# Kernel optimization log

Measured on AMD Instinct MI355X. Metric: run time of the kernel, lower is better.

The kernel has to match this reference:

```python
import jax, jax.numpy as jnp
import numpy as np

B, L, D, H, A = 4, 2048, 1024, 16, 64  # batch, seq, d_model, n_head, d_head


def setup_inputs() -> dict:
    key = jax.random.key(0)
    ks = jax.random.split(key, 6)
    scale = 1.0 / np.sqrt(D)
    return {
        "xq": jax.random.normal(ks[0], (B, L, D), dtype=jnp.float32),
        "xkv": jax.random.normal(ks[1], (B, L, D), dtype=jnp.float32),
        "Q": jax.random.normal(ks[2], (D, H, A), dtype=jnp.float32) * scale,
        "K": jax.random.normal(ks[3], (D, H, A), dtype=jnp.float32) * scale,
        "V": jax.random.normal(ks[4], (D, H, A), dtype=jnp.float32) * scale,
        "O": jax.random.normal(ks[5], (D, H, A), dtype=jnp.float32) * scale,
    }


def reference(xq, xkv, Q, K, V, O):
    # embed: 'dha, ...ld -> ...lha'
    q = jnp.einsum('dha,bld->blha', Q, xq)
    k = jnp.einsum('dha,bld->blha', K, xkv)
    v = jnp.einsum('dha,bld->blha', V, xkv)
    # outer: '...lha, ...mha -> ...hlm'  (full LxL score matrix, no scaling in source)
    scores = jnp.einsum('blha,bmha->bhlm', q, k)
    attn = jax.nn.softmax(scores, axis=-1)  # dropout p=0 (eval)
    # score: '...hlm, ...mha -> ...lha'
    ctx = jnp.einsum('bhlm,bmha->blha', attn, v)
    # output: '...dha, ...lha -> ...ld'
    return jnp.einsum('dha,blha->bld', O, ctx)
```

## Files before the change

### kernel.cpp

```cpp
#include <hip/hip_runtime.h>
#include <math.h>

typedef __bf16 bf16;
typedef bf16 bf16x8 __attribute__((ext_vector_type(8)));
typedef bf16 bf16x4 __attribute__((ext_vector_type(4)));
typedef float f32x4 __attribute__((ext_vector_type(4)));
typedef float f32x16 __attribute__((ext_vector_type(16)));

#define B_ 4
#define L_ 2048
#define D_ 1024
#define H_ 16
#define A_ 64
#define HA_ 1024
#define BL_ 8192
#define LOG2E 1.44269504088896340736f

__device__ __forceinline__ void gload16(const void* g, void* l) {
  __builtin_amdgcn_global_load_lds((const __attribute__((address_space(1))) void*)g,
                                   (__attribute__((address_space(3))) void*)l,
                                   16, 0, 0);
}

__device__ __forceinline__ unsigned cvt_pk_bf16(float lo, float hi) {
  unsigned r;
  asm volatile("v_cvt_pk_bf16_f32 %0, %1, %2" : "=v"(r) : "v"(lo), "v"(hi));
  return r;
}

__device__ __forceinline__ void permswap(unsigned& a, unsigned& b) {
  asm volatile("v_permlane32_swap_b32 %0, %1" : "+v"(a), "+v"(b));
}

__global__ __launch_bounds__(256) void cast_f32_bf16(const float* __restrict__ src,
                                                     bf16* __restrict__ dst, int n8) {
  int i = blockIdx.x * blockDim.x + threadIdx.x;
  if (i >= n8) return;
  const float4* s = reinterpret_cast<const float4*>(src) + (size_t)i * 2;
  float4 a = s[0], b = s[1];
  bf16x8 o;
  o[0] = (bf16)a.x; o[1] = (bf16)a.y; o[2] = (bf16)a.z; o[3] = (bf16)a.w;
  o[4] = (bf16)b.x; o[5] = (bf16)b.y; o[6] = (bf16)b.z; o[7] = (bf16)b.w;
  *reinterpret_cast<bf16x8*>(dst + (size_t)i * 8) = o;
}

__global__ __launch_bounds__(256) void transpose_cast_w(const float* __restrict__ w,
                                                        bf16* __restrict__ wt, float scale) {
  __shared__ float tile[32][33];
  const int d0 = blockIdx.y * 32, h0 = blockIdx.x * 32;
  const int tx = threadIdx.x, ty = threadIdx.y;
  #pragma unroll
  for (int j = 0; j < 4; j++)
    tile[ty + j * 8][tx] = w[(size_t)(d0 + ty + j * 8) * HA_ + h0 + tx];
  __syncthreads();
  #pragma unroll
  for (int j = 0; j < 4; j++)
    wt[(size_t)(h0 + ty + j * 8) * D_ + d0 + tx] = (bf16)(tile[tx][ty + j * 8] * scale);
}

__global__ __launch_bounds__(256) void transpose_v(const bf16* __restrict__ vb,
                                                   bf16* __restrict__ vtb) {
  __shared__ bf16 tile[64][72];
  const int bh = blockIdx.y;
  const int l0 = blockIdx.x * 64;
  const bf16* src = vb + (size_t)bh * L_ * A_ + (size_t)l0 * A_;
  bf16* dst = vtb + (size_t)bh * A_ * L_ + l0;
  const int tid = threadIdx.x;
  {
    int r = tid >> 2, cs = (tid & 3) * 16;
    bf16x8 v0 = *reinterpret_cast<const bf16x8*>(src + r * 64 + cs);
    bf16x8 v1 = *reinterpret_cast<const bf16x8*>(src + r * 64 + cs + 8);
    #pragma unroll
    for (int j = 0; j < 8; j++) { tile[r][cs + j] = v0[j]; tile[r][cs + 8 + j] = v1[j]; }
  }
  __syncthreads();
  {
    int a = tid >> 2, ls = (tid & 3) * 16;
    bf16x8 o0, o1;
    #pragma unroll
    for (int j = 0; j < 8; j++) { o0[j] = tile[ls + j][a]; o1[j] = tile[ls + 8 + j][a]; }
    *reinterpret_cast<bf16x8*>(dst + (size_t)a * L_ + ls) = o0;
    *reinterpret_cast<bf16x8*>(dst + (size_t)a * L_ + ls + 8) = o1;
  }
}

template <int MODE>
__device__ __forceinline__ void gemm_bt_core(const bf16* __restrict__ Ap,
                                             const bf16* __restrict__ Bp,
                                             void* __restrict__ Cp) {
  const int K = 1024;
  __shared__ __align__(16) bf16 As[128 * 32];
  __shared__ __align__(16) bf16 Bs[128 * 32];
  const int tid = threadIdx.x;
  const int m0 = blockIdx.y * 128, n0 = blockIdx.x * 128;
  const int lane = tid & 63, w = tid >> 6;
  const int wr = w >> 1, wc = w & 1;
  const int g = lane >> 4, c = lane & 15;
  f32x4 acc[4][4] = {};
  const int srow = tid >> 2, sch = tid & 3;
  const int sw0 = (sch ^ (srow & 3)) * 8;
  for (int k0 = 0; k0 < K; k0 += 32) {
    gload16(Ap + (size_t)(m0 + srow) * K + k0 + sw0, As + tid * 8);
    gload16(Ap + (size_t)(m0 + 64 + srow) * K + k0 + sw0, As + (256 + tid) * 8);
    gload16(Bp + (size_t)(n0 + srow) * K + k0 + sw0, Bs + tid * 8);
    gload16(Bp + (size_t)(n0 + 64 + srow) * K + k0 + sw0, Bs + (256 + tid) * 8);
    __syncthreads();
    bf16x8 af[4], bfr[4];
    #pragma unroll
    for (int m = 0; m < 4; m++)
      af[m] = *reinterpret_cast<const bf16x8*>(As + (wr * 64 + m * 16 + c) * 32 + ((g ^ (c & 3)) * 8));
    #pragma unroll
    for (int n = 0; n < 4; n++)
      bfr[n] = *reinterpret_cast<const bf16x8*>(Bs + (wc * 64 + n * 16 + c) * 32 + ((g ^ (c & 3)) * 8));
    #pragma unroll
    for (int m = 0; m < 4; m++)
      #pragma unroll
      for (int n = 0; n < 4; n++)
        acc[m][n] = __builtin_amdgcn_mfma_f32_16x16x32_bf16(af[m], bfr[n], acc[m][n], 0, 0, 0);
    __syncthreads();
  }
  #pragma unroll
  for (int m = 0; m < 4; m++) {
    #pragma unroll
    for (int n = 0; n < 4; n++) {
      #pragma unroll
      for (int i = 0; i < 4; i++) {
        int row = m0 + wr * 64 + m * 16 + g * 4 + i;
        int col = n0 + wc * 64 + n * 16 + c;
        float v = acc[m][n][i];
        if (MODE == 0) {
          int b = row >> 11, l = row & 2047, h = col >> 6, a = col & 63;
          ((bf16*)Cp)[(((size_t)b * H_ + h) * L_ + l) * A_ + a] = (bf16)v;
        } else {
          ((float*)Cp)[(size_t)row * 1024 + col] = v;
        }
      }
    }
  }
}

__global__ __launch_bounds__(256, 2) void gemm_proj(const bf16* xq_b, const bf16* xkv_b,
                                                    const bf16* wq, const bf16* wk, const bf16* wv,
                                                    bf16* qb, bf16* kb, bf16* vb) {
  const int z = blockIdx.z;
  const bf16* Ap = (z == 0) ? xq_b : xkv_b;
  const bf16* Bp = (z == 0) ? wq : (z == 1) ? wk : wv;
  bf16* Cp = (z == 0) ? qb : (z == 1) ? kb : vb;
  gemm_bt_core<0>(Ap, Bp, Cp);
}

__global__ __launch_bounds__(256, 2) void gemm_out_k(const bf16* ctx, const bf16* wo, float* out) {
  gemm_bt_core<1>(ctx, wo, out);
}

__device__ __forceinline__ void pa_build(const f32x16& s, bf16x8& f0, bf16x8& f1) {
  #pragma unroll
  for (int sl = 0; sl < 2; sl++) {
    unsigned a0 = cvt_pk_bf16(s[8 * sl + 0], s[8 * sl + 1]);
    unsigned b0 = cvt_pk_bf16(s[8 * sl + 4], s[8 * sl + 5]);
    permswap(a0, b0);
    unsigned a1 = cvt_pk_bf16(s[8 * sl + 2], s[8 * sl + 3]);
    unsigned b1 = cvt_pk_bf16(s[8 * sl + 6], s[8 * sl + 7]);
    permswap(a1, b1);
    uint4 v; v.x = a0; v.y = a1; v.z = b0; v.w = b1;
    if (sl == 0) f0 = __builtin_bit_cast(bf16x8, v);
    else         f1 = __builtin_bit_cast(bf16x8, v);
  }
}

__global__ __launch_bounds__(512, 2) void attn_kernel(const bf16* __restrict__ qg,
                                                      const bf16* __restrict__ kg,
                                                      const bf16* __restrict__ vtg,
                                                      bf16* __restrict__ ctx) {
  __shared__ __align__(16) bf16 Ks[2][64 * 64];
  __shared__ __align__(16) bf16 Vs[2][64 * 64];
  const int tid = threadIdx.x;
  const int lane = tid & 63;
  const int w = tid >> 6;
  const int c = lane & 31;
  const int hi = lane >> 5;
  const int cs7 = c & 7;
  const int bh = blockIdx.y;
  const int q0 = blockIdx.x * 256;
  const bf16* qh = qg + (size_t)bh * L_ * A_;
  const bf16* kh = kg + (size_t)bh * L_ * A_;
  const bf16* vh = vtg + (size_t)bh * A_ * L_;

  const int qrow = q0 + w * 32 + c;
  bf16x8 qf[4];
  #pragma unroll
  for (int ds = 0; ds < 4; ds++)
    qf[ds] = *reinterpret_cast<const bf16x8*>(qh + (size_t)qrow * A_ + ds * 16 + hi * 8);

  f32x16 oacc0 = {}, oacc1 = {};
  float mrun = -INFINITY, lrun = 0.f;

  auto stage = [&](int buf, int tile) {
    const int kv0 = tile * 64;
    int r = tid >> 3, s = tid & 7;
    int ss = (s ^ (r & 7)) * 8;
    gload16(kh + (size_t)(kv0 + r) * A_ + ss, &Ks[buf][tid * 8]);
    gload16(vh + (size_t)r * L_ + kv0 + ss, &Vs[buf][tid * 8]);
  };

  stage(0, 0);
  __syncthreads();
  int cur = 0;

  for (int t = 0; t < L_ / 64; t++) {
    if (t < L_ / 64 - 1) stage(cur ^ 1, t + 1);
    const bf16* Kc = Ks[cur];
    const bf16* Vc = Vs[cur];

    f32x16 s0 = {}, s1 = {};
    __builtin_amdgcn_s_setprio(1);
    #pragma unroll
    for (int ds = 0; ds < 4; ds++) {
      bf16x8 k0 = *reinterpret_cast<const bf16x8*>(Kc + (size_t)c * 64 + ((2 * ds + hi) ^ cs7) * 8);
      bf16x8 k1 = *reinterpret_cast<const bf16x8*>(Kc + (size_t)(32 + c) * 64 + ((2 * ds + hi) ^ cs7) * 8);
      s0 = __builtin_amdgcn_mfma_f32_32x32x16_bf16(k0, qf[ds], s0, 0, 0, 0);
      s1 = __builtin_amdgcn_mfma_f32_32x32x16_bf16(k1, qf[ds], s1, 0, 0, 0);
    }
    __builtin_amdgcn_s_setprio(0);

    float t0[8];
    #pragma unroll
    for (int r = 0; r < 8; r++)
      t0[r] = fmaxf(fmaxf(s0[r], s0[r + 8]), fmaxf(s1[r], s1[r + 8]));
    float t1 = fmaxf(fmaxf(fmaxf(t0[0], t0[1]), fmaxf(t0[2], t0[3])),
                     fmaxf(fmaxf(t0[4], t0[5]), fmaxf(t0[6], t0[7])));
    float pmax = fmaxf(t1, __shfl_xor(t1, 32));

    if (!__all(pmax <= mrun + 8.f)) {
      float mn = fmaxf(mrun, pmax);
      float sc = __builtin_amdgcn_exp2f(mrun - mn);
      lrun *= sc;
      #pragma unroll
      for (int r = 0; r < 16; r++) { oacc0[r] *= sc; oacc1[r] *= sc; }
      mrun = mn;
    }

    #pragma unroll
    for (int r = 0; r < 16; r++) {
      s0[r] = __builtin_amdgcn_exp2f(s0[r] - mrun);
      s1[r] = __builtin_amdgcn_exp2f(s1[r] - mrun);
    }

    float u0[8];
    #pragma unroll
    for (int r = 0; r < 8; r++)
      u0[r] = (s0[r] + s0[r + 8]) + (s1[r] + s1[r + 8]);
    float us = ((u0[0] + u0[1]) + (u0[2] + u0[3])) + ((u0[4] + u0[5]) + (u0[6] + u0[7]));
    lrun += us + __shfl_xor(us, 32);

    bf16x8 paf0, paf1, paf2, paf3;
    pa_build(s0, paf0, paf1);
    pa_build(s1, paf2, paf3);

    __builtin_amdgcn_s_setprio(1);
    #pragma unroll
    for (int ks = 0; ks < 4; ks++) {
      const bf16x8 pa = (ks == 0) ? paf0 : (ks == 1) ? paf1 : (ks == 2) ? paf2 : paf3;
      bf16x8 v0 = *reinterpret_cast<const bf16x8*>(Vc + (size_t)c * 64 + ((2 * ks + hi) ^ cs7) * 8);
      bf16x8 v1 = *reinterpret_cast<const bf16x8*>(Vc + (size_t)(32 + c) * 64 + ((2 * ks + hi) ^ cs7) * 8);
      oacc0 = __builtin_amdgcn_mfma_f32_32x32x16_bf16(v0, pa, oacc0, 0, 0, 0);
      oacc1 = __builtin_amdgcn_mfma_f32_32x32x16_bf16(v1, pa, oacc1, 0, 0, 0);
    }
    __builtin_amdgcn_s_setprio(0);

    __syncthreads();
    cur ^= 1;
  }

  float inv = 1.f / lrun;
  const int b = bh >> 4, h = bh & 15;
  bf16* crow = ctx + (((size_t)b * L_ + qrow) * H_ + h) * A_;
  #pragma unroll
  for (int n = 0; n < 2; n++) {
    #pragma unroll
    for (int rq = 0; rq < 4; rq++) {
      bf16x4 o4;
      #pragma unroll
      for (int j = 0; j < 4; j++) {
        float v = (n == 0) ? oacc0[rq * 4 + j] : oacc1[rq * 4 + j];
        o4[j] = (bf16)(v * inv);
      }
      *reinterpret_cast<bf16x4*>(crow + n * 32 + rq * 8 + hi * 4) = o4;
    }
  }
}

extern "C" void kernel_launch(void* const* d_in, const int* in_sizes, int n_in,
                              void* d_out, int out_size, void* d_ws, size_t ws_size,
                              hipStream_t stream) {
  const float* xq = (const float*)d_in[0];
  const float* xkv = (const float*)d_in[1];
  const float* Qw = (const float*)d_in[2];
  const float* Kw = (const float*)d_in[3];
  const float* Vw = (const float*)d_in[4];
  const float* Ow = (const float*)d_in[5];
  float* out = (float*)d_out;

  char* ws = (char*)d_ws;
  const size_t SZ16 = (size_t)BL_ * HA_ * sizeof(bf16);
  const size_t SZW = (size_t)D_ * HA_ * sizeof(bf16);
  bf16* xq_b = (bf16*)(ws);
  bf16* xkv_b = (bf16*)(ws + SZ16);
  bf16* wq_t = (bf16*)(ws + 2 * SZ16);
  bf16* wk_t = (bf16*)(ws + 2 * SZ16 + SZW);
  bf16* wv_t = (bf16*)(ws + 2 * SZ16 + 2 * SZW);
  bf16* wo_b = (bf16*)(ws + 2 * SZ16 + 3 * SZW);
  bf16* qb = (bf16*)(ws + 2 * SZ16 + 4 * SZW);
  bf16* kb = qb + (size_t)BL_ * HA_;
  bf16* vb = kb + (size_t)BL_ * HA_;
  bf16* vtb = xq_b;
  bf16* ctxb = xkv_b;

  cast_f32_bf16<<<4096, 256, 0, stream>>>(xq, xq_b, BL_ * D_ / 8);
  cast_f32_bf16<<<4096, 256, 0, stream>>>(xkv, xkv_b, BL_ * D_ / 8);
  cast_f32_bf16<<<512, 256, 0, stream>>>(Ow, wo_b, D_ * HA_ / 8);
  dim3 tb(32, 8);
  transpose_cast_w<<<dim3(32, 32), tb, 0, stream>>>(Qw, wq_t, LOG2E);
  transpose_cast_w<<<dim3(32, 32), tb, 0, stream>>>(Kw, wk_t, 1.0f);
  transpose_cast_w<<<dim3(32, 32), tb, 0, stream>>>(Vw, wv_t, 1.0f);

  gemm_proj<<<dim3(8, 64, 3), 256, 0, stream>>>(xq_b, xkv_b, wq_t, wk_t, wv_t, qb, kb, vb);
  transpose_v<<<dim3(32, 64), 256, 0, stream>>>(vb, vtb);
  attn_kernel<<<dim3(8, 64), 512, 0, stream>>>(qb, kb, vtb, ctxb);
  gemm_out_k<<<dim3(8, 64), 256, 0, stream>>>(ctxb, wo_b, out);
}
```

Measured before the change: 236.9 us.

## Fold running max into score accumulator init and swap grid dimension order

Result: faster. 217.9 us (-8.0%).

```diff
diff --git a/kernel.cpp b/kernel.cpp
--- a/kernel.cpp
+++ b/kernel.cpp
@@ -30,6 +30,14 @@
 
 __device__ __forceinline__ void permswap(unsigned& a, unsigned& b) {
   asm volatile("v_permlane32_swap_b32 %0, %1" : "+v"(a), "+v"(b));
+}
+
+__device__ __forceinline__ void half_pair(float x, float& o1, float& o2) {
+  unsigned a = __builtin_bit_cast(unsigned, x), b;
+  asm volatile("v_mov_b32 %0, %1" : "=v"(b) : "v"(a));
+  asm volatile("v_permlane32_swap_b32 %0, %1" : "+v"(a), "+v"(b));
+  o1 = __builtin_bit_cast(float, a);
+  o2 = __builtin_bit_cast(float, b);
 }
 
 __global__ __launch_bounds__(256) void cast_f32_bf16(const float* __restrict__ src,
@@ -92,7 +100,7 @@
   __shared__ __align__(16) bf16 As[128 * 32];
   __shared__ __align__(16) bf16 Bs[128 * 32];
   const int tid = threadIdx.x;
-  const int m0 = blockIdx.y * 128, n0 = blockIdx.x * 128;
+  const int m0 = blockIdx.x * 128, n0 = blockIdx.y * 128;
   const int lane = tid & 63, w = tid >> 6;
   const int wr = w >> 1, wc = w & 1;
   const int g = lane >> 4, c = lane & 15;
@@ -180,8 +188,8 @@
   const int c = lane & 31;
   const int hi = lane >> 5;
   const int cs7 = c & 7;
-  const int bh = blockIdx.y;
-  const int q0 = blockIdx.x * 256;
+  const int bh = blockIdx.x;
+  const int q0 = blockIdx.y * 256;
   const bf16* qh = qg + (size_t)bh * L_ * A_;
   const bf16* kh = kg + (size_t)bh * L_ * A_;
   const bf16* vh = vtg + (size_t)bh * A_ * L_;
@@ -193,7 +201,7 @@
     qf[ds] = *reinterpret_cast<const bf16x8*>(qh + (size_t)qrow * A_ + ds * 16 + hi * 8);
 
   f32x16 oacc0 = {}, oacc1 = {};
-  float mrun = -INFINITY, lrun = 0.f;
+  float mrun = 0.f, lrun = 0.f;
 
   auto stage = [&](int buf, int tile) {
     const int kv0 = tile * 64;
@@ -212,7 +220,10 @@
     const bf16* Kc = Ks[cur];
     const bf16* Vc = Vs[cur];
 
-    f32x16 s0 = {}, s1 = {};
+    f32x16 s0, s1;
+    const float nm = -mrun;
+    #pragma unroll
+    for (int r = 0; r < 16; r++) { s0[r] = nm; s1[r] = nm; }
     __builtin_amdgcn_s_setprio(1);
     #pragma unroll
     for (int ds = 0; ds < 4; ds++) {
@@ -226,24 +237,28 @@
     float t0[8];
     #pragma unroll
     for (int r = 0; r < 8; r++)
-      t0[r] = fmaxf(fmaxf(s0[r], s0[r + 8]), fmaxf(s1[r], s1[r + 8]));
+      t0[r] = fmaxf(fmaxf(fmaxf(s0[r], s0[r + 8]), s1[r]), s1[r + 8]);
     float t1 = fmaxf(fmaxf(fmaxf(t0[0], t0[1]), fmaxf(t0[2], t0[3])),
                      fmaxf(fmaxf(t0[4], t0[5]), fmaxf(t0[6], t0[7])));
-    float pmax = fmaxf(t1, __shfl_xor(t1, 32));
-
-    if (!__all(pmax <= mrun + 8.f)) {
-      float mn = fmaxf(mrun, pmax);
-      float sc = __builtin_amdgcn_exp2f(mrun - mn);
+    float x1, x2;
+    half_pair(t1, x1, x2);
+    float pmax = fmaxf(x1, x2);
+
+    if (!__all(pmax <= 8.f)) {
+      float d = fmaxf(pmax, 0.f);
+      float sc = __builtin_amdgcn_exp2f(-d);
       lrun *= sc;
       #pragma unroll
       for (int r = 0; r < 16; r++) { oacc0[r] *= sc; oacc1[r] *= sc; }
-      mrun = mn;
+      mrun += d;
+      #pragma unroll
+      for (int r = 0; r < 16; r++) { s0[r] -= d; s1[r] -= d; }
     }
 
     #pragma unroll
     for (int r = 0; r < 16; r++) {
-      s0[r] = __builtin_amdgcn_exp2f(s0[r] - mrun);
-      s1[r] = __builtin_amdgcn_exp2f(s1[r] - mrun);
+      s0[r] = __builtin_amdgcn_exp2f(s0[r]);
+      s1[r] = __builtin_amdgcn_exp2f(s1[r]);
     }
 
     float u0[8];
@@ -251,7 +266,9 @@
     for (int r = 0; r < 8; r++)
       u0[r] = (s0[r] + s0[r + 8]) + (s1[r] + s1[r + 8]);
     float us = ((u0[0] + u0[1]) + (u0[2] + u0[3])) + ((u0[4] + u0[5]) + (u0[6] + u0[7]));
-    lrun += us + __shfl_xor(us, 32);
+    float y1, y2;
+    half_pair(us, y1, y2);
+    lrun += y1 + y2;
 
     bf16x8 paf0, paf1, paf2, paf3;
     pa_build(s0, paf0, paf1);
@@ -324,8 +341,8 @@
   transpose_cast_w<<<dim3(32, 32), tb, 0, stream>>>(Kw, wk_t, 1.0f);
   transpose_cast_w<<<dim3(32, 32), tb, 0, stream>>>(Vw, wv_t, 1.0f);
 
-  gemm_proj<<<dim3(8, 64, 3), 256, 0, stream>>>(xq_b, xkv_b, wq_t, wk_t, wv_t, qb, kb, vb);
+  gemm_proj<<<dim3(64, 8, 3), 256, 0, stream>>>(xq_b, xkv_b, wq_t, wk_t, wv_t, qb, kb, vb);
   transpose_v<<<dim3(32, 64), 256, 0, stream>>>(vb, vtb);
-  attn_kernel<<<dim3(8, 64), 512, 0, stream>>>(qb, kb, vtb, ctxb);
-  gemm_out_k<<<dim3(8, 64), 256, 0, stream>>>(ctxb, wo_b, out);
-}
+  attn_kernel<<<dim3(64, 8), 512, 0, stream>>>(qb, kb, vtb, ctxb);
+  gemm_out_k<<<dim3(64, 8), 256, 0, stream>>>(ctxb, wo_b, out);
+}
```
